# Performance work log

Measured on AMD Instinct MI355X. Metric: run time of the kernel, lower is better.

Reference implementation:

```python
import jax, jax.numpy as jnp
import numpy as np


def setup_inputs() -> dict:
    key = jax.random.key(0)
    ks = jax.random.split(key, 9)
    B, Cin, H, W = 16, 512, 64, 64
    Cout = 256
    s_in = 0.02  # small init scale for stable softmax
    return {
        "x": jax.random.normal(ks[0], (B, Cin, H, W), dtype=jnp.float32),
        "Wq": jax.random.normal(ks[1], (Cout, Cin), dtype=jnp.float32) * s_in,
        "bq": jnp.zeros((Cout,), dtype=jnp.float32),
        "Wk": jax.random.normal(ks[2], (Cout, Cin), dtype=jnp.float32) * s_in,
        "bk": jnp.zeros((Cout,), dtype=jnp.float32),
        "Wv": jax.random.normal(ks[3], (Cout, Cin), dtype=jnp.float32) * s_in,
        "bv": jnp.zeros((Cout,), dtype=jnp.float32),
        "Wo": jax.random.normal(ks[4], (Cin, Cout), dtype=jnp.float32) * s_in,
        "bo": jnp.zeros((Cin,), dtype=jnp.float32),
    }


def reference(x, Wq, bq, Wk, bk, Wv, bv, Wo, bo):
    B, C, H, W = x.shape
    N = H * W
    xf = x.reshape(B, C, N)  # flatten spatial
    # 1x1 convs == per-pixel linear maps over channels
    q = jnp.einsum('oc,bcn->bon', Wq, xf) + bq[None, :, None]  # [B,Cout,N]
    k = jnp.einsum('oc,bcn->bon', Wk, xf) + bk[None, :, None]
    v = jnp.einsum('oc,bcn->bon', Wv, xf) + bv[None, :, None]
    # NOTE: original contracts over spatial dim N -> channel-attention [B,Cout,Cout]
    scale = jnp.asarray(N, x.dtype) ** 0.5  # query.size(-1) == N
    scores = jnp.einsum('bcn,bdn->bcd', q, k) / scale
    attn = jax.nn.softmax(scores, axis=-1)  # softmax over key-channel dim
    out = jnp.einsum('bcd,bdn->bcn', attn, v)  # [B,Cout,N]
    # permute(0,2,1).view(B,-1,H,W): row-major reshape of (B,N,Cout)
    out = jnp.transpose(out, (0, 2, 1)).reshape(B, -1, H, W)  # [B,Cout,H,W]
    out = jnp.einsum('co,bohw->bchw', Wo, out) + bo[None, :, None, None]
    return out
```

## Files before the change

### kernel.cpp

```cpp
#include <hip/hip_runtime.h>
#include <math.h>

typedef unsigned short u16;
typedef __bf16 bf16x8 __attribute__((ext_vector_type(8)));
typedef float f32x4 __attribute__((ext_vector_type(4)));
typedef unsigned short u16x4 __attribute__((ext_vector_type(4)));
typedef unsigned short u16x8 __attribute__((ext_vector_type(8)));

__device__ __forceinline__ u16 f2bf(float f) {
    unsigned int u = __float_as_uint(f);
    return (u16)((u + 0x7FFF + ((u >> 16) & 1)) >> 16);
}

#define BAR() do { __builtin_amdgcn_sched_barrier(0); __builtin_amdgcn_s_barrier(); __builtin_amdgcn_sched_barrier(0); } while (0)

__device__ __forceinline__ void stage_half(
    const u16* __restrict__ g, int ld, int row0, int rstride, int kt,
    u16* lds, int w, int l)
{
    #pragma unroll
    for (int qq = 0; qq < 2; ++qq) {
        const int c0 = qq * 512 + w * 64;
        const int c  = c0 + l;
        const int r  = c >> 3, kc = c & 7;
        const int kcg = kc ^ (r & 7);
        const u16* src = g + (size_t)(row0 + r * rstride) * ld + kt + kcg * 8;
        __builtin_amdgcn_global_load_lds(
            (const __attribute__((address_space(1))) unsigned int*)src,
            (__attribute__((address_space(3))) unsigned int*)(lds + (size_t)c0 * 8),
            16, 0, 0);
    }
}

#define QUAD(q_) do {                                                          \
    bf16x8 af0[2], af1[2];                                                     \
    { int row = wm + ((q_) * 2 + 0) * 16 + p;                                  \
      af0[0] = *(const bf16x8*)(bufA + row * 64 + ((0 + g) ^ (row & 7)) * 8);  \
      af0[1] = *(const bf16x8*)(bufA + row * 64 + ((4 + g) ^ (row & 7)) * 8); }\
    { int row = wm + ((q_) * 2 + 1) * 16 + p;                                  \
      af1[0] = *(const bf16x8*)(bufA + row * 64 + ((0 + g) ^ (row & 7)) * 8);  \
      af1[1] = *(const bf16x8*)(bufA + row * 64 + ((4 + g) ^ (row & 7)) * 8); }\
    __builtin_amdgcn_s_setprio(1);                                             \
    _Pragma("unroll")                                                          \
    for (int nf = 0; nf < 4; ++nf) {                                           \
        acc[(q_)*2+0][nf] = __builtin_amdgcn_mfma_f32_16x16x32_bf16(af0[0], bfr[nf][0], acc[(q_)*2+0][nf], 0, 0, 0); \
        acc[(q_)*2+0][nf] = __builtin_amdgcn_mfma_f32_16x16x32_bf16(af0[1], bfr[nf][1], acc[(q_)*2+0][nf], 0, 0, 0); \
        acc[(q_)*2+1][nf] = __builtin_amdgcn_mfma_f32_16x16x32_bf16(af1[0], bfr[nf][0], acc[(q_)*2+1][nf], 0, 0, 0); \
        acc[(q_)*2+1][nf] = __builtin_amdgcn_mfma_f32_16x16x32_bf16(af1[1], bfr[nf][1], acc[(q_)*2+1][nf], 0, 0, 0); \
    }                                                                          \
    __builtin_amdgcn_s_setprio(0);                                             \
} while (0)

template<int NT>
__device__ __forceinline__ void gemm256(
    const u16* __restrict__ Ag, int ldA, int baseA, int rsA,
    const u16* __restrict__ Bg, int ldB, int n0,
    u16* sm, f32x4 (&acc)[8][4])
{
    const int tid = threadIdx.x;
    const int l = tid & 63, w = tid >> 6;
    const int p = l & 15, g = l >> 4;
    const int wm = (w >> 2) * 128;
    const int wn = (w & 3) * 64;

    stage_half(Ag, ldA, baseA,             rsA, 0, sm,         w, l);
    stage_half(Ag, ldA, baseA + 128 * rsA, rsA, 0, sm + 8192,  w, l);
    stage_half(Bg, ldB, n0,       1, 0, sm + 16384, w, l);
    stage_half(Bg, ldB, n0 + 128, 1, 0, sm + 24576, w, l);

    for (int t = 0; t < NT; ++t) {
        u16* bufA  = sm + (t & 1) * 32768;
        u16* bufB  = bufA + 16384;
        u16* nbufA = sm + ((t + 1) & 1) * 32768;
        u16* nbufB = nbufA + 16384;
        const int kt1 = (t + 1) * 64;

        if (t + 1 < NT) {
            stage_half(Ag, ldA, baseA,             rsA, kt1, nbufA,        w, l);
            stage_half(Ag, ldA, baseA + 128 * rsA, rsA, kt1, nbufA + 8192, w, l);
            asm volatile("s_waitcnt vmcnt(4)" ::: "memory");
        } else {
            asm volatile("s_waitcnt vmcnt(0)" ::: "memory");
        }
        BAR();
        bf16x8 bfr[4][2];
        #pragma unroll
        for (int nf = 0; nf < 4; ++nf) {
            int row = wn + nf * 16 + p;
            bfr[nf][0] = *(const bf16x8*)(bufB + row * 64 + ((0 + g) ^ (row & 7)) * 8);
            bfr[nf][1] = *(const bf16x8*)(bufB + row * 64 + ((4 + g) ^ (row & 7)) * 8);
        }
        QUAD(0);
        BAR();
        if (t + 1 < NT) stage_half(Bg, ldB, n0, 1, kt1, nbufB, w, l);
        QUAD(1);
        BAR();
        if (t + 1 < NT) stage_half(Bg, ldB, n0 + 128, 1, kt1, nbufB + 8192, w, l);
        QUAD(2);
        BAR();
        QUAD(3);
        BAR();
    }
}

__global__ __launch_bounds__(256) void k0_prep(
    const float* __restrict__ x, u16* __restrict__ xT,
    const float* __restrict__ Wq, const float* __restrict__ Wk,
    const float* __restrict__ Wv, const float* __restrict__ Wo,
    u16* __restrict__ wqk, u16* __restrict__ wv, u16* __restrict__ wo)
{
    const int tid = threadIdx.x;
    if (blockIdx.z == 16) {
        const int bid = blockIdx.y * 64 + blockIdx.x;
        const int sel = bid >> 7;
        const int sub = bid & 127;
        const float* s = sel == 0 ? Wq : sel == 1 ? Wk : sel == 2 ? Wv : Wo;
        u16* d = sel == 0 ? wqk : sel == 1 ? (wqk + 131072) : sel == 2 ? wv : wo;
        int i = (sub * 256 + tid) * 4;
        float4 v = *(const float4*)(s + i);
        u16x4 u = {f2bf(v.x), f2bf(v.y), f2bf(v.z), f2bf(v.w)};
        *(u16x4*)(d + i) = u;
        return;
    }
    __shared__ float Tx[64 * 65];
    const int b = blockIdx.z, c0 = blockIdx.y * 64, n0 = blockIdx.x * 64;
    const float* xb = x + (size_t)b * 512 * 4096;
    #pragma unroll
    for (int r = 0; r < 4; ++r) {
        int crow = (tid >> 4) + r * 16;
        int ncol = (tid & 15) * 4;
        float4 v = *(const float4*)(xb + (size_t)(c0 + crow) * 4096 + n0 + ncol);
        Tx[(ncol + 0) * 65 + crow] = v.x;
        Tx[(ncol + 1) * 65 + crow] = v.y;
        Tx[(ncol + 2) * 65 + crow] = v.z;
        Tx[(ncol + 3) * 65 + crow] = v.w;
    }
    __syncthreads();
    u16* ob = xT + (size_t)b * 4096 * 512;
    #pragma unroll
    for (int cc = 0; cc < 2; ++cc) {
        int id = cc * 256 + tid;
        int nrow = id >> 3;
        int cch = (id & 7) * 8;
        u16x8 u;
        #pragma unroll
        for (int j = 0; j < 8; ++j) u[j] = f2bf(Tx[nrow * 65 + cch + j]);
        *(u16x8*)(ob + (size_t)(n0 + nrow) * 512 + c0 + cch) = u;
    }
}

__global__ __launch_bounds__(512, 2) void k1_qkv(
    const u16* __restrict__ wqk, const u16* __restrict__ wv,
    const float* __restrict__ bq, const float* __restrict__ bk, const float* __restrict__ bv,
    const u16* __restrict__ xT, u16* __restrict__ q, u16* __restrict__ kmat,
    u16* __restrict__ vT)
{
    __shared__ u16 sm[65536];
    const int b = blockIdx.z;
    const int y = blockIdx.y;
    const u16* xb = xT + (size_t)b * 4096 * 512;

    const int tid = threadIdx.x;
    const int l = tid & 63, w = tid >> 6;
    const int p = l & 15, g = l >> 4;
    const int wm = (w >> 2) * 128, wn = (w & 3) * 64;

    f32x4 acc[8][4] = {};

    if (y < 2) {
        const int m0 = y * 256;
        const int n0 = blockIdx.x * 256;
        gemm256<8>(wqk, 512, m0, 1, xb, 512, n0, sm, acc);

        const float* bias = (y == 0) ? bq : bk;
        u16* outp = ((y == 0) ? q : kmat) + ((size_t)b << 20);
        #pragma unroll
        for (int mf = 0; mf < 8; ++mf)
            #pragma unroll
            for (int nf = 0; nf < 4; ++nf) {
                int n = n0 + wn + nf * 16 + p;
                #pragma unroll
                for (int r = 0; r < 4; ++r) {
                    int mloc = wm + mf * 16 + g * 4 + r;
                    outp[(size_t)mloc * 4096 + n] = f2bf(acc[mf][nf][r] + bias[mloc]);
                }
            }
    } else {
        const int m0 = blockIdx.x * 256;
        gemm256<8>(xb, 512, m0, 1, wv, 512, 0, sm, acc);

        u16* outp = vT + ((size_t)b << 20);
        #pragma unroll
        for (int nf = 0; nf < 4; ++nf) {
            int d = wn + nf * 16 + p;
            float bvv = bv[d];
            #pragma unroll
            for (int mf = 0; mf < 8; ++mf) {
                #pragma unroll
                for (int r = 0; r < 4; ++r) {
                    int row = m0 + wm + mf * 16 + g * 4 + r;
                    outp[(size_t)row * 256 + d] = f2bf(acc[mf][nf][r] + bvv);
                }
            }
        }
    }
}

__global__ __launch_bounds__(512, 2) void k2_scores(
    const u16* __restrict__ q, const u16* __restrict__ kmat, float* __restrict__ spart)
{
    __shared__ u16 sm[65536];
    const int b = blockIdx.z;
    const int split = blockIdx.x;
    const u16* A = q    + ((size_t)b << 20) + split * 256;
    const u16* B = kmat + ((size_t)b << 20) + split * 256;

    f32x4 acc[8][4] = {};
    gemm256<4>(A, 4096, 0, 1, B, 4096, 0, sm, acc);

    const int tid = threadIdx.x;
    const int l = tid & 63, w = tid >> 6;
    const int p = l & 15, g = l >> 4;
    const int wm = (w >> 2) * 128, wn = (w & 3) * 64;

    float* sp = spart + ((size_t)split * 16 + b) * 65536;
    #pragma unroll
    for (int mf = 0; mf < 8; ++mf)
        #pragma unroll
        for (int nf = 0; nf < 4; ++nf) {
            int n = wn + nf * 16 + p;
            #pragma unroll
            for (int r = 0; r < 4; ++r) {
                int m = wm + mf * 16 + g * 4 + r;
                sp[(size_t)m * 256 + n] = acc[mf][nf][r] * 0.015625f;
            }
        }
}

__global__ __launch_bounds__(256) void k3_softmax(
    const float* __restrict__ sp, u16* __restrict__ attn)
{
    const int row = blockIdx.x;
    const int tid = threadIdx.x;
    const size_t STRIDE = (size_t)16 * 65536;
    const size_t base = (size_t)row * 256 + tid;

    float s = 0.f;
    #pragma unroll
    for (int i = 0; i < 16; ++i) s += sp[base + i * STRIDE];

    __shared__ float red[4];
    float m = s;
    #pragma unroll
    for (int off = 32; off >= 1; off >>= 1) m = fmaxf(m, __shfl_xor(m, off));
    if ((tid & 63) == 0) red[tid >> 6] = m;
    __syncthreads();
    m = fmaxf(fmaxf(red[0], red[1]), fmaxf(red[2], red[3]));

    float e = expf(s - m);
    float t = e;
    #pragma unroll
    for (int off = 32; off >= 1; off >>= 1) t += __shfl_xor(t, off);
    __syncthreads();
    if ((tid & 63) == 0) red[tid >> 6] = t;
    __syncthreads();
    t = red[0] + red[1] + red[2] + red[3];

    attn[base] = f2bf(e / t);
}

__global__ __launch_bounds__(512, 2) void k4_pv(
    const u16* __restrict__ attn, const u16* __restrict__ vT, u16* __restrict__ outT3)
{
    __shared__ u16 sm[65536];
    const int b  = blockIdx.z;
    const int sh = blockIdx.x;
    const u16* A = vT   + ((size_t)b << 20);
    const u16* B = attn + ((size_t)b << 16);

    f32x4 acc[8][4] = {};
    gemm256<4>(A, 256, sh, 16, B, 256, 0, sm, acc);

    const int tid = threadIdx.x;
    const int l = tid & 63, w = tid >> 6;
    const int p = l & 15, g = l >> 4;
    const int wm = (w >> 2) * 128, wn = (w & 3) * 64;

    u16* outp = outT3 + (((size_t)b * 16 + sh) << 16);
    #pragma unroll
    for (int mf = 0; mf < 8; ++mf)
        #pragma unroll
        for (int nf = 0; nf < 4; ++nf) {
            int co  = wn + nf * 16 + p;
            int nh0 = wm + mf * 16 + g * 4;
            u16x4 u = {f2bf(acc[mf][nf][0]), f2bf(acc[mf][nf][1]),
                       f2bf(acc[mf][nf][2]), f2bf(acc[mf][nf][3])};
            *(u16x4*)(outp + (size_t)co * 256 + nh0) = u;
        }
}

__global__ __launch_bounds__(512, 2) void k5_final(
    const u16* __restrict__ wo, const float* __restrict__ bo,
    const u16* __restrict__ outT3, float* __restrict__ out)
{
    __shared__ u16 sm[65536];
    const int bz = blockIdx.z;
    const int b  = bz >> 4, sh = bz & 15;
    const int m0 = blockIdx.y * 256;
    const u16* B = outT3 + ((size_t)bz << 16);

    f32x4 acc[8][4] = {};
    gemm256<4>(wo, 256, m0, 1, B, 256, 0, sm, acc);

    const int tid = threadIdx.x;
    const int l = tid & 63, w = tid >> 6;
    const int p = l & 15, g = l >> 4;
    const int wm = (w >> 2) * 128, wn = (w & 3) * 64;

    float* ob = out + (size_t)b * 2097152 + (size_t)sh * 256;
    #pragma unroll
    for (int mf = 0; mf < 8; ++mf)
        #pragma unroll
        for (int nf = 0; nf < 4; ++nf) {
            int slo = wn + nf * 16 + p;
            #pragma unroll
            for (int r = 0; r < 4; ++r) {
                int m = m0 + wm + mf * 16 + g * 4 + r;
                ob[(size_t)m * 4096 + slo] = acc[mf][nf][r] + bo[m];
            }
        }
}

extern "C" void kernel_launch(void* const* d_in, const int* in_sizes, int n_in,
                              void* d_out, int out_size, void* d_ws, size_t ws_size,
                              hipStream_t stream) {
    (void)in_sizes; (void)n_in; (void)out_size; (void)ws_size;
    const float* x  = (const float*)d_in[0];
    const float* Wq = (const float*)d_in[1];
    const float* bq = (const float*)d_in[2];
    const float* Wk = (const float*)d_in[3];
    const float* bk = (const float*)d_in[4];
    const float* Wv = (const float*)d_in[5];
    const float* bv = (const float*)d_in[6];
    const float* Wo = (const float*)d_in[7];
    const float* bo = (const float*)d_in[8];
    float* out = (float*)d_out;

    char* ws = (char*)d_ws;
    u16* xT   = (u16*)(ws + 0);
    u16* q    = (u16*)(ws + 67108864);
    u16* kmat = (u16*)(ws + 100663296);
    u16* vT   = (u16*)(ws + 134217728);
    float* spart = (float*)(ws + 0);
    u16* attn    = (u16*)(ws + 67108864);
    u16* outT3   = (u16*)(ws + 100663296);
    u16* wqk  = (u16*)(ws + 167772160);
    u16* wv   = (u16*)(ws + 168296448);
    u16* wo   = (u16*)(ws + 168558592);

    k0_prep   <<<dim3(64, 8, 17), dim3(256), 0, stream>>>(x, xT, Wq, Wk, Wv, Wo, wqk, wv, wo);
    k1_qkv    <<<dim3(16, 3, 16), dim3(512), 0, stream>>>(wqk, wv, bq, bk, bv, xT, q, kmat, vT);
    k2_scores <<<dim3(16, 1, 16), dim3(512), 0, stream>>>(q, kmat, spart);
    k3_softmax<<<dim3(4096),      dim3(256), 0, stream>>>(spart, attn);
    k4_pv     <<<dim3(16, 1, 16), dim3(512), 0, stream>>>(attn, vT, outT3);
    k5_final  <<<dim3(1, 2, 256), dim3(512), 0, stream>>>(wo, bo, outT3, out);
}
```

Baseline: 200.4 us.

## Switch GEMM mainloop to 4-stage K=32 LDS pipeline and halve score split-K

Replaces the double-buffered K=64 tile loop with a four-buffer ring of K=32 tiles, prefetching three tiles ahead with graded vmcnt waits, and drops the XOR swizzle so loads are plain row-major. Each iteration now issues fewer barriers, loading A fragments in two halves. Separately, the scores kernel uses 8 split-K chunks of 512 instead of 16 of 256, and softmax sums 8 partials. Risks include LDS bank conflicts from the unswizzled 64-byte rows and less parallelism in the scores kernel.

```diff
diff --git a/kernel.cpp b/kernel.cpp
--- a/kernel.cpp
+++ b/kernel.cpp
@@ -14,7 +14,7 @@
 
 #define BAR() do { __builtin_amdgcn_sched_barrier(0); __builtin_amdgcn_s_barrier(); __builtin_amdgcn_sched_barrier(0); } while (0)
 
-__device__ __forceinline__ void stage_half(
+__device__ __forceinline__ void stg(
     const u16* __restrict__ g, int ld, int row0, int rstride, int kt,
     u16* lds, int w, int l)
 {
@@ -22,34 +22,13 @@
     for (int qq = 0; qq < 2; ++qq) {
         const int c0 = qq * 512 + w * 64;
         const int c  = c0 + l;
-        const int r  = c >> 3, kc = c & 7;
-        const int kcg = kc ^ (r & 7);
-        const u16* src = g + (size_t)(row0 + r * rstride) * ld + kt + kcg * 8;
+        const u16* src = g + (size_t)(row0 + (c >> 2) * rstride) * ld + kt + (c & 3) * 8;
         __builtin_amdgcn_global_load_lds(
             (const __attribute__((address_space(1))) unsigned int*)src,
             (__attribute__((address_space(3))) unsigned int*)(lds + (size_t)c0 * 8),
             16, 0, 0);
     }
 }
-
-#define QUAD(q_) do {                                                          \
-    bf16x8 af0[2], af1[2];                                                     \
-    { int row = wm + ((q_) * 2 + 0) * 16 + p;                                  \
-      af0[0] = *(const bf16x8*)(bufA + row * 64 + ((0 + g) ^ (row & 7)) * 8);  \
-      af0[1] = *(const bf16x8*)(bufA + row * 64 + ((4 + g) ^ (row & 7)) * 8); }\
-    { int row = wm + ((q_) * 2 + 1) * 16 + p;                                  \
-      af1[0] = *(const bf16x8*)(bufA + row * 64 + ((0 + g) ^ (row & 7)) * 8);  \
-      af1[1] = *(const bf16x8*)(bufA + row * 64 + ((4 + g) ^ (row & 7)) * 8); }\
-    __builtin_amdgcn_s_setprio(1);                                             \
-    _Pragma("unroll")                                                          \
-    for (int nf = 0; nf < 4; ++nf) {                                           \
-        acc[(q_)*2+0][nf] = __builtin_amdgcn_mfma_f32_16x16x32_bf16(af0[0], bfr[nf][0], acc[(q_)*2+0][nf], 0, 0, 0); \
-        acc[(q_)*2+0][nf] = __builtin_amdgcn_mfma_f32_16x16x32_bf16(af0[1], bfr[nf][1], acc[(q_)*2+0][nf], 0, 0, 0); \
-        acc[(q_)*2+1][nf] = __builtin_amdgcn_mfma_f32_16x16x32_bf16(af1[0], bfr[nf][0], acc[(q_)*2+1][nf], 0, 0, 0); \
-        acc[(q_)*2+1][nf] = __builtin_amdgcn_mfma_f32_16x16x32_bf16(af1[1], bfr[nf][1], acc[(q_)*2+1][nf], 0, 0, 0); \
-    }                                                                          \
-    __builtin_amdgcn_s_setprio(0);                                             \
-} while (0)
 
 template<int NT>
 __device__ __forceinline__ void gemm256(
@@ -63,42 +42,65 @@
     const int wm = (w >> 2) * 128;
     const int wn = (w & 3) * 64;
 
-    stage_half(Ag, ldA, baseA,             rsA, 0, sm,         w, l);
-    stage_half(Ag, ldA, baseA + 128 * rsA, rsA, 0, sm + 8192,  w, l);
-    stage_half(Bg, ldB, n0,       1, 0, sm + 16384, w, l);
-    stage_half(Bg, ldB, n0 + 128, 1, 0, sm + 24576, w, l);
-
+    #pragma unroll
+    for (int t = 0; t < 3; ++t) {
+        u16* buf = sm + (t & 3) * 16384;
+        stg(Ag, ldA, baseA, rsA, t * 32, buf, w, l);
+        stg(Bg, ldB, n0, 1, t * 32, buf + 8192, w, l);
+    }
+
+    #pragma unroll
     for (int t = 0; t < NT; ++t) {
-        u16* bufA  = sm + (t & 1) * 32768;
-        u16* bufB  = bufA + 16384;
-        u16* nbufA = sm + ((t + 1) & 1) * 32768;
-        u16* nbufB = nbufA + 16384;
-        const int kt1 = (t + 1) * 64;
-
-        if (t + 1 < NT) {
-            stage_half(Ag, ldA, baseA,             rsA, kt1, nbufA,        w, l);
-            stage_half(Ag, ldA, baseA + 128 * rsA, rsA, kt1, nbufA + 8192, w, l);
-            asm volatile("s_waitcnt vmcnt(4)" ::: "memory");
-        } else {
-            asm volatile("s_waitcnt vmcnt(0)" ::: "memory");
+        u16* bufA = sm + (t & 3) * 16384;
+        u16* bufB = bufA + 8192;
+        u16* nbuf = sm + ((t + 3) & 3) * 16384;
+
+        if (t + 3 < NT) stg(Ag, ldA, baseA, rsA, (t + 3) * 32, nbuf, w, l);
+        {
+            const int r = NT - 1 - t;
+            if (r >= 3)      asm volatile("s_waitcnt vmcnt(10)" ::: "memory");
+            else if (r == 2) asm volatile("s_waitcnt vmcnt(8)"  ::: "memory");
+            else if (r == 1) asm volatile("s_waitcnt vmcnt(4)"  ::: "memory");
+            else             asm volatile("s_waitcnt vmcnt(0)"  ::: "memory");
         }
         BAR();
-        bf16x8 bfr[4][2];
+        bf16x8 bfr[4];
         #pragma unroll
         for (int nf = 0; nf < 4; ++nf) {
             int row = wn + nf * 16 + p;
-            bfr[nf][0] = *(const bf16x8*)(bufB + row * 64 + ((0 + g) ^ (row & 7)) * 8);
-            bfr[nf][1] = *(const bf16x8*)(bufB + row * 64 + ((4 + g) ^ (row & 7)) * 8);
-        }
-        QUAD(0);
-        BAR();
-        if (t + 1 < NT) stage_half(Bg, ldB, n0, 1, kt1, nbufB, w, l);
-        QUAD(1);
-        BAR();
-        if (t + 1 < NT) stage_half(Bg, ldB, n0 + 128, 1, kt1, nbufB + 8192, w, l);
-        QUAD(2);
-        BAR();
-        QUAD(3);
+            bfr[nf] = *(const bf16x8*)(bufB + row * 32 + g * 8);
+        }
+        {
+            bf16x8 af[4];
+            #pragma unroll
+            for (int i = 0; i < 4; ++i) {
+                int row = wm + i * 16 + p;
+                af[i] = *(const bf16x8*)(bufA + row * 32 + g * 8);
+            }
+            __builtin_amdgcn_s_setprio(1);
+            #pragma unroll
+            for (int i = 0; i < 4; ++i)
+                #pragma unroll
+                for (int nf = 0; nf < 4; ++nf)
+                    acc[i][nf] = __builtin_amdgcn_mfma_f32_16x16x32_bf16(af[i], bfr[nf], acc[i][nf], 0, 0, 0);
+            __builtin_amdgcn_s_setprio(0);
+        }
+        if (t + 3 < NT) stg(Bg, ldB, n0, 1, (t + 3) * 32, nbuf + 8192, w, l);
+        {
+            bf16x8 af[4];
+            #pragma unroll
+            for (int i = 0; i < 4; ++i) {
+                int row = wm + (4 + i) * 16 + p;
+                af[i] = *(const bf16x8*)(bufA + row * 32 + g * 8);
+            }
+            __builtin_amdgcn_s_setprio(1);
+            #pragma unroll
+            for (int i = 0; i < 4; ++i)
+                #pragma unroll
+                for (int nf = 0; nf < 4; ++nf)
+                    acc[4 + i][nf] = __builtin_amdgcn_mfma_f32_16x16x32_bf16(af[i], bfr[nf], acc[4 + i][nf], 0, 0, 0);
+            __builtin_amdgcn_s_setprio(0);
+        }
         BAR();
     }
 }
@@ -170,7 +172,7 @@
     if (y < 2) {
         const int m0 = y * 256;
         const int n0 = blockIdx.x * 256;
-        gemm256<8>(wqk, 512, m0, 1, xb, 512, n0, sm, acc);
+        gemm256<16>(wqk, 512, m0, 1, xb, 512, n0, sm, acc);
 
         const float* bias = (y == 0) ? bq : bk;
         u16* outp = ((y == 0) ? q : kmat) + ((size_t)b << 20);
@@ -187,7 +189,7 @@
             }
     } else {
         const int m0 = blockIdx.x * 256;
-        gemm256<8>(xb, 512, m0, 1, wv, 512, 0, sm, acc);
+        gemm256<16>(xb, 512, m0, 1, wv, 512, 0, sm, acc);
 
         u16* outp = vT + ((size_t)b << 20);
         #pragma unroll
@@ -212,11 +214,11 @@
     __shared__ u16 sm[65536];
     const int b = blockIdx.z;
     const int split = blockIdx.x;
-    const u16* A = q    + ((size_t)b << 20) + split * 256;
-    const u16* B = kmat + ((size_t)b << 20) + split * 256;
+    const u16* A = q    + ((size_t)b << 20) + split * 512;
+    const u16* B = kmat + ((size_t)b << 20) + split * 512;
 
     f32x4 acc[8][4] = {};
-    gemm256<4>(A, 4096, 0, 1, B, 4096, 0, sm, acc);
+    gemm256<16>(A, 4096, 0, 1, B, 4096, 0, sm, acc);
 
     const int tid = threadIdx.x;
     const int l = tid & 63, w = tid >> 6;
@@ -247,7 +249,7 @@
 
     float s = 0.f;
     #pragma unroll
-    for (int i = 0; i < 16; ++i) s += sp[base + i * STRIDE];
+    for (int i = 0; i < 8; ++i) s += sp[base + i * STRIDE];
 
     __shared__ float red[4];
     float m = s;
@@ -279,7 +281,7 @@
     const u16* B = attn + ((size_t)b << 16);
 
     f32x4 acc[8][4] = {};
-    gemm256<4>(A, 256, sh, 16, B, 256, 0, sm, acc);
+    gemm256<8>(A, 256, sh, 16, B, 256, 0, sm, acc);
 
     const int tid = threadIdx.x;
     const int l = tid & 63, w = tid >> 6;
@@ -310,7 +312,7 @@
     const u16* B = outT3 + ((size_t)bz << 16);
 
     f32x4 acc[8][4] = {};
-    gemm256<4>(wo, 256, m0, 1, B, 256, 0, sm, acc);
+    gemm256<8>(wo, 256, m0, 1, B, 256, 0, sm, acc);
 
     const int tid = threadIdx.x;
     const int l = tid & 63, w = tid >> 6;
@@ -360,7 +362,7 @@
 
     k0_prep   <<<dim3(64, 8, 17), dim3(256), 0, stream>>>(x, xT, Wq, Wk, Wv, Wo, wqk, wv, wo);
     k1_qkv    <<<dim3(16, 3, 16), dim3(512), 0, stream>>>(wqk, wv, bq, bk, bv, xT, q, kmat, vT);
-    k2_scores <<<dim3(16, 1, 16), dim3(512), 0, stream>>>(q, kmat, spart);
+    k2_scores <<<dim3(8, 1, 16),  dim3(512), 0, stream>>>(q, kmat, spart);
     k3_softmax<<<dim3(4096),      dim3(256), 0, stream>>>(spart, attn);
     k4_pv     <<<dim3(16, 1, 16), dim3(512), 0, stream>>>(attn, vT, outT3);
     k5_final  <<<dim3(1, 2, 256), dim3(512), 0, stream>>>(wo, bo, outT3, out);
```

Result: no change. 198.8 us (-0.8%).
